# Kernel tuning notes

Hardware: AMD Instinct MI355X
Metric: run time of the kernel (lower is better)

The kernel has to match this reference:

```python
import jax, jax.numpy as jnp
import numpy as np

# Config constants from the W-Net paper (Config() in the original repo)
RADIUS = 5.0
SIGMA_X = 4.0
SIGMA_I = 10.0
PAD = 5  # window offsets dm, dn in [-5, 4] (torch.arange exclusive upper bound)

# Precompute the static list of active window offsets.
# Original: if dist < radius -> w = 0; else w = (dist^2 / -sigma_x) * (||dx|| / -sigma_i)
# (the two negatives cancel, so w = dist^2/sigma_x * ||dx||/sigma_i).
_OFFSETS = []
for dm in range(-5, 5):
    for dn in range(-5, 5):
        d2 = dm * dm + dn * dn
        if np.sqrt(d2) >= RADIUS:  # NOTE: faithful to the (inverted-looking) source condition
            _OFFSETS.append((dm, dn, d2 / SIGMA_X))


def setup_inputs() -> dict:
    key = jax.random.key(0)
    k1, k2 = jax.random.split(key)
    N, K, X, Y, C = 8, 20, 224, 224, 3
    seg = jax.random.uniform(k1, (N, K, X, Y), dtype=jnp.float32)
    x = jax.random.uniform(k2, (N, C, X, Y), dtype=jnp.float32)
    return {"seg": seg, "x": x}


def reference(seg, x):
    N, K, X, Y = seg.shape
    Kconst = jnp.float32(K)
    xi = jnp.transpose(x, (0, 2, 3, 1))  # [N, X, Y, C], matches x[idx].transpose(0,2).transpose(0,1)

    # Zero padding: out-of-window pixels get seg=0, killing their contribution,
    # which exactly reproduces the max(0,.)/min(X,.) loop bounds.
    xp = jnp.pad(xi, ((0, 0), (PAD, PAD), (PAD, PAD), (0, 0)))
    sp = jnp.pad(seg, ((0, 0), (0, 0), (PAD, PAD), (PAD, PAD)))

    # assocA[n,k,i,j] = seg[n,k,i,j] * sum_{dm,dn} w(i,j,i+dm,j+dn) * seg[n,k,i+dm,j+dn]
    accA = jnp.zeros((N, K), dtype=seg.dtype)
    for dm, dn, sw in _OFFSETS:  # static, ~31 offsets
        xs = jax.lax.dynamic_slice(xp, (0, PAD + dm, PAD + dn, 0), (N, X, Y, xi.shape[-1]))
        ss = jax.lax.dynamic_slice(sp, (0, 0, PAD + dm, PAD + dn), (N, K, X, Y))
        diffn = jnp.linalg.norm(xi - xs, axis=-1)  # [N, X, Y], ||xi[i,j]-xi[m,n]||_2
        w = (jnp.float32(sw)) * (diffn / jnp.float32(SIGMA_I))  # [N, X, Y]
        accA = accA + jnp.sum(seg * (w[:, None] * ss), axis=(2, 3))
    assocA_sum = accA  # [N, K]

    # assocV[n,k,i,j] = seg[n,k,i,j] * sum_{m,n'} ||xi[i,j] - xi[m,n']||^2
    # expand: XY*||xi[i,j]||^2 - 2 xi[i,j].S + sum ||xi||^2
    sq = jnp.sum(xi * xi, axis=-1)               # [N, X, Y]
    s2 = jnp.sum(sq, axis=(1, 2))                # [N]
    S = jnp.sum(xi, axis=(1, 2))                 # [N, C]
    npix = jnp.float32(X * Y)
    temp = npix * sq - 2.0 * jnp.einsum('nxyc,nc->nxy', xi, S) + s2[:, None, None]
    assocV_sum = jnp.einsum('nkxy,nxy->nk', seg, temp)  # [N, K]

    Nassoc = assocA_sum / assocV_sum             # [N, K]
    loss = jnp.sum(Kconst - jnp.sum(Nassoc, axis=1))  # sum over batch
    return loss.reshape(1)
```

## Files before the change

kernel.cpp:

```cpp
#include <hip/hip_runtime.h>

#define NB 8
#define KK 20
#define XD 224
#define YD 224
#define NPIX (XD*YD)
#define TILE 16
#define NT 14
#define TW 26
#define NOFF 31
#define NKTOT (NB*KK)
#define NTILES (NT*NT)
#define NPH 2
#define KPH 10
#define SB 32

namespace {
constexpr int DM[NOFF] = {
  -5,-5,-5,-5,-5,-5,-5,-5,-5,-5,
  -4,-4,-4,-4,-4,
  -3,-3,-3,
  -2,-1, 0, 1, 2,
   3, 3, 3,
   4, 4, 4, 4, 4};
constexpr int DN[NOFF] = {
  -5,-4,-3,-2,-1, 0, 1, 2, 3, 4,
  -5,-4,-3, 3, 4,
  -5,-4, 4,
  -5,-5,-5,-5,-5,
  -5,-4, 4,
  -5,-4,-3, 3, 4};

constexpr int ROFXI[NOFF] = {
  (DM[0]+5)*TW+(DN[0]+5),  (DM[1]+5)*TW+(DN[1]+5),  (DM[2]+5)*TW+(DN[2]+5),
  (DM[3]+5)*TW+(DN[3]+5),  (DM[4]+5)*TW+(DN[4]+5),  (DM[5]+5)*TW+(DN[5]+5),
  (DM[6]+5)*TW+(DN[6]+5),  (DM[7]+5)*TW+(DN[7]+5),  (DM[8]+5)*TW+(DN[8]+5),
  (DM[9]+5)*TW+(DN[9]+5),  (DM[10]+5)*TW+(DN[10]+5),(DM[11]+5)*TW+(DN[11]+5),
  (DM[12]+5)*TW+(DN[12]+5),(DM[13]+5)*TW+(DN[13]+5),(DM[14]+5)*TW+(DN[14]+5),
  (DM[15]+5)*TW+(DN[15]+5),(DM[16]+5)*TW+(DN[16]+5),(DM[17]+5)*TW+(DN[17]+5),
  (DM[18]+5)*TW+(DN[18]+5),(DM[19]+5)*TW+(DN[19]+5),(DM[20]+5)*TW+(DN[20]+5),
  (DM[21]+5)*TW+(DN[21]+5),(DM[22]+5)*TW+(DN[22]+5),(DM[23]+5)*TW+(DN[23]+5),
  (DM[24]+5)*TW+(DN[24]+5),(DM[25]+5)*TW+(DN[25]+5),(DM[26]+5)*TW+(DN[26]+5),
  (DM[27]+5)*TW+(DN[27]+5),(DM[28]+5)*TW+(DN[28]+5),(DM[29]+5)*TW+(DN[29]+5),
  (DM[30]+5)*TW+(DN[30]+5)};
constexpr float COSC[NOFF] = {
  (DM[0]*DM[0]+DN[0]*DN[0])/40.0f,   (DM[1]*DM[1]+DN[1]*DN[1])/40.0f,
  (DM[2]*DM[2]+DN[2]*DN[2])/40.0f,   (DM[3]*DM[3]+DN[3]*DN[3])/40.0f,
  (DM[4]*DM[4]+DN[4]*DN[4])/40.0f,   (DM[5]*DM[5]+DN[5]*DN[5])/40.0f,
  (DM[6]*DM[6]+DN[6]*DN[6])/40.0f,   (DM[7]*DM[7]+DN[7]*DN[7])/40.0f,
  (DM[8]*DM[8]+DN[8]*DN[8])/40.0f,   (DM[9]*DM[9]+DN[9]*DN[9])/40.0f,
  (DM[10]*DM[10]+DN[10]*DN[10])/40.0f,(DM[11]*DM[11]+DN[11]*DN[11])/40.0f,
  (DM[12]*DM[12]+DN[12]*DN[12])/40.0f,(DM[13]*DM[13]+DN[13]*DN[13])/40.0f,
  (DM[14]*DM[14]+DN[14]*DN[14])/40.0f,(DM[15]*DM[15]+DN[15]*DN[15])/40.0f,
  (DM[16]*DM[16]+DN[16]*DN[16])/40.0f,(DM[17]*DM[17]+DN[17]*DN[17])/40.0f,
  (DM[18]*DM[18]+DN[18]*DN[18])/40.0f,(DM[19]*DM[19]+DN[19]*DN[19])/40.0f,
  (DM[20]*DM[20]+DN[20]*DN[20])/40.0f,(DM[21]*DM[21]+DN[21]*DN[21])/40.0f,
  (DM[22]*DM[22]+DN[22]*DN[22])/40.0f,(DM[23]*DM[23]+DN[23]*DN[23])/40.0f,
  (DM[24]*DM[24]+DN[24]*DN[24])/40.0f,(DM[25]*DM[25]+DN[25]*DN[25])/40.0f,
  (DM[26]*DM[26]+DN[26]*DN[26])/40.0f,(DM[27]*DM[27]+DN[27]*DN[27])/40.0f,
  (DM[28]*DM[28]+DN[28]*DN[28])/40.0f,(DM[29]*DM[29]+DN[29]*DN[29])/40.0f,
  (DM[30]*DM[30]+DN[30]*DN[30])/40.0f};
}

__global__ void ncuts_stats1(const float* __restrict__ x, float* __restrict__ part) {
  __shared__ float red[4][4];
  const int b = blockIdx.x;
  const int n = b >> 5, s = b & 31;
  const int t = threadIdx.x;
  const int lane = t & 63, wv = t >> 6;
  const float* xb = x + n * 3 * NPIX;
  const int base = s * (NPIX / SB);
  float a0 = 0.f, a1 = 0.f, a2 = 0.f, aq = 0.f;
  for (int i = t; i < NPIX / SB; i += 256) {
    const int p = base + i;
    float v0 = xb[p], v1 = xb[NPIX + p], v2 = xb[2 * NPIX + p];
    a0 += v0; a1 += v1; a2 += v2;
    aq = fmaf(v0, v0, fmaf(v1, v1, fmaf(v2, v2, aq)));
  }
  #pragma unroll
  for (int m = 1; m < 64; m <<= 1) {
    a0 += __shfl_xor(a0, m, 64); a1 += __shfl_xor(a1, m, 64);
    a2 += __shfl_xor(a2, m, 64); aq += __shfl_xor(aq, m, 64);
  }
  if (lane == 0) { red[wv][0] = a0; red[wv][1] = a1; red[wv][2] = a2; red[wv][3] = aq; }
  __syncthreads();
  if (t < 4) part[b * 4 + t] = red[0][t] + red[1][t] + red[2][t] + red[3][t];
}

__global__ void ncuts_stats2(const float* __restrict__ part,
                             float* __restrict__ Sv, float* __restrict__ s2v) {
  const int t = threadIdx.x;
  if (t < NB * 4) {
    const int n = t >> 2, val = t & 3;
    float s = 0.f;
    #pragma unroll 4
    for (int i = 0; i < SB; ++i) s += part[(n * SB + i) * 4 + val];
    if (val < 3) Sv[n * 3 + val] = s; else s2v[n] = s;
  }
}

__global__ __launch_bounds__(256, 4)
void ncuts_main(const float* __restrict__ seg, const float* __restrict__ x,
                const float* __restrict__ Sv, const float* __restrict__ s2v,
                float* __restrict__ pA, float* __restrict__ pV) {
  __shared__ __align__(16) float sSegA[TW*TW*4];
  __shared__ __align__(16) float sSegB[TW*TW*4];
  __shared__ __align__(16) float sSegC[TW*TW*2];
  __shared__ __align__(16) float sXi[TW*TW*4];
  __shared__ float sRed[4][2*KK];

  const int t = threadIdx.x;
  const int lane = t & 63, wv = t >> 6;
  const int tx = t & 15, ty = t >> 4;
  const int tcx = blockIdx.x, tcy = blockIdx.y, n = blockIdx.z;
  const int r0 = tcy * TILE - 5, c0 = tcx * TILE - 5;

  const float* xb = x + n * 3 * NPIX;
  for (int e = t; e < TW * TW; e += 256) {
    const int rr = e / TW, cc = e - rr * TW;
    const int gr = r0 + rr, gc = c0 + cc;
    float v0 = 0.f, v1 = 0.f, v2 = 0.f;
    if ((unsigned)gr < XD && (unsigned)gc < YD) {
      const int g = gr * YD + gc;
      v0 = xb[g]; v1 = xb[NPIX + g]; v2 = xb[2 * NPIX + g];
    }
    *reinterpret_cast<float4*>(&sXi[e * 4]) = make_float4(v0, v1, v2, 0.f);
  }

  const float* sb = seg + n * KK * NPIX;
  const float* psb[3]; bool pok[3];
  #pragma unroll
  for (int s = 0; s < 3; ++s) {
    const int p = t + s * 256;
    const int rr = p / TW, cc = p - rr * TW;
    const int gr = r0 + rr, gc = c0 + cc;
    pok[s] = (p < TW * TW) && ((unsigned)gr < XD) && ((unsigned)gc < YD);
    psb[s] = sb + (gr * YD + gc);
  }

  const int xib = ty * TW + tx;
  const int cen = xib + (5 * TW + 5);

  const float S0 = Sv[n*3+0], S1 = Sv[n*3+1], S2 = Sv[n*3+2], s2n = s2v[n];

  __syncthreads();
  const float4 xc = *reinterpret_cast<const float4*>(&sXi[cen * 4]);
  const float xc0 = xc.x, xc1 = xc.y, xc2 = xc.z;
  const float sqc = xc0*xc0 + xc1*xc1 + xc2*xc2;
  const float temp = 50176.f * sqc - 2.f * (xc0*S0 + xc1*S1 + xc2*S2) + s2n;

  #pragma unroll 1
  for (int p = 0; p < NPH; ++p) {
    const int kbase = p * KPH;

    __syncthreads();

    #pragma unroll
    for (int s = 0; s < 3; ++s) {
      const int pix = t + s * 256;
      if (pix < TW * TW) {
        float v[KPH];
        #pragma unroll
        for (int ks = 0; ks < KPH; ++ks) v[ks] = 0.f;
        if (pok[s]) {
          #pragma unroll
          for (int ks = 0; ks < KPH; ++ks) v[ks] = psb[s][(kbase + ks) * NPIX];
        }
        *reinterpret_cast<float4*>(&sSegA[pix * 4]) = make_float4(v[0], v[1], v[2], v[3]);
        *reinterpret_cast<float4*>(&sSegB[pix * 4]) = make_float4(v[4], v[5], v[6], v[7]);
        *reinterpret_cast<float2*>(&sSegC[pix * 2]) = make_float2(v[8], v[9]);
      }
    }
    __syncthreads();

    float acc[KPH];
    #pragma unroll
    for (int k = 0; k < KPH; ++k) acc[k] = 0.f;

    #pragma unroll 2
    for (int o = 0; o < NOFF; ++o) {
      const int rof = ROFXI[o];
      const float4 xs = *reinterpret_cast<const float4*>(&sXi[(xib + rof) * 4]);
      const float d0 = xc0 - xs.x, d1 = xc1 - xs.y, d2 = xc2 - xs.z;
      const float dd = fmaf(d0, d0, fmaf(d1, d1, d2 * d2));
      const float w = COSC[o] * dd * __frsqrt_rn(fmaxf(dd, 1e-30f));
      const float4 q0 = *reinterpret_cast<const float4*>(&sSegA[(xib + rof) * 4]);
      const float4 q1 = *reinterpret_cast<const float4*>(&sSegB[(xib + rof) * 4]);
      const float2 q2 = *reinterpret_cast<const float2*>(&sSegC[(xib + rof) * 2]);
      acc[0] = fmaf(w, q0.x, acc[0]); acc[1] = fmaf(w, q0.y, acc[1]);
      acc[2] = fmaf(w, q0.z, acc[2]); acc[3] = fmaf(w, q0.w, acc[3]);
      acc[4] = fmaf(w, q1.x, acc[4]); acc[5] = fmaf(w, q1.y, acc[5]);
      acc[6] = fmaf(w, q1.z, acc[6]); acc[7] = fmaf(w, q1.w, acc[7]);
      acc[8] = fmaf(w, q2.x, acc[8]); acc[9] = fmaf(w, q2.y, acc[9]);
    }

    const float4 c0v = *reinterpret_cast<const float4*>(&sSegA[cen * 4]);
    const float4 c1v = *reinterpret_cast<const float4*>(&sSegB[cen * 4]);
    const float2 c2v = *reinterpret_cast<const float2*>(&sSegC[cen * 2]);
    const float segc[KPH] = {c0v.x, c0v.y, c0v.z, c0v.w,
                             c1v.x, c1v.y, c1v.z, c1v.w, c2v.x, c2v.y};

    #pragma unroll
    for (int pp = 0; pp < KPH / 2; ++pp) {
      const int s0i = 2 * pp, s1i = 2 * pp + 1;
      float pa0 = segc[s0i] * acc[s0i], pv0 = segc[s0i] * temp;
      float pa1 = segc[s1i] * acc[s1i], pv1 = segc[s1i] * temp;
      float s0 = (lane & 1) ? pv0 : pa0;
      float g0 = (lane & 1) ? pa0 : pv0;
      s0 += __shfl_xor(g0, 1, 64);
      float s1 = (lane & 1) ? pv1 : pa1;
      float g1 = (lane & 1) ? pa1 : pv1;
      s1 += __shfl_xor(g1, 1, 64);
      float cv = (lane & 2) ? s1 : s0;
      float gv = (lane & 2) ? s0 : s1;
      cv += __shfl_xor(gv, 2, 64);
      cv += __shfl_xor(cv, 4, 64);
      cv += __shfl_xor(cv, 8, 64);
      cv += __shfl_xor(cv, 16, 64);
      cv += __shfl_xor(cv, 32, 64);
      const int k0g = kbase + 2 * pp;
      if (lane < 4) sRed[wv][2 * k0g + lane] = cv;
    }
  }

  __syncthreads();
  if (t < 2 * KK) {
    const float s = sRed[0][t] + sRed[1][t] + sRed[2][t] + sRed[3][t];
    const int tile = tcy * NT + tcx;
    const int k = t >> 1;
    float* dst = (t & 1) ? pV : pA;
    dst[(n * KK + k) * NTILES + tile] = s;
  }
}

__global__ void ncuts_final1(const float* __restrict__ pA, const float* __restrict__ pV,
                             float* __restrict__ rA, float* __restrict__ rV) {
  const int nk = blockIdx.x, t = threadIdx.x;
  float a = 0.f, v = 0.f;
  for (int j = t; j < NTILES; j += 64) {
    a += pA[nk * NTILES + j];
    v += pV[nk * NTILES + j];
  }
  #pragma unroll
  for (int m = 1; m < 64; m <<= 1) {
    a += __shfl_xor(a, m, 64);
    v += __shfl_xor(v, m, 64);
  }
  if (t == 0) { rA[nk] = a; rV[nk] = v; }
}

__global__ void ncuts_final2(const float* __restrict__ rA, const float* __restrict__ rV,
                             float* __restrict__ out) {
  __shared__ float red[256];
  const int t = threadIdx.x;
  float r = 0.f;
  if (t < NKTOT) r = rA[t] / rV[t];
  red[t] = r;
  __syncthreads();
  for (int s = 128; s > 0; s >>= 1) {
    if (t < s) red[t] += red[t + s];
    __syncthreads();
  }
  if (t == 0) out[0] = (float)NKTOT - red[0];
}

extern "C" void kernel_launch(void* const* d_in, const int* in_sizes, int n_in,
                              void* d_out, int out_size, void* d_ws, size_t ws_size,
                              hipStream_t stream) {
  const float* seg = (const float*)d_in[0];
  const float* x   = (const float*)d_in[1];
  float* ws   = (float*)d_ws;
  float* pA   = ws;
  float* pV   = ws + NKTOT * NTILES;
  float* Sv   = ws + 2 * NKTOT * NTILES;
  float* s2v  = Sv + 24;
  float* part = s2v + 8;
  float* rA   = part + 1024;
  float* rV   = rA + NKTOT;

  ncuts_stats1<<<NB * SB, 256, 0, stream>>>(x, part);
  ncuts_stats2<<<1, 64, 0, stream>>>(part, Sv, s2v);
  dim3 grid(NT, NT, NB);
  ncuts_main<<<grid, 256, 0, stream>>>(seg, x, Sv, s2v, pA, pV);
  ncuts_final1<<<NKTOT, 64, 0, stream>>>(pA, pV, rA, rV);
  ncuts_final2<<<1, 256, 0, stream>>>(rA, rV, (float*)d_out);
}
```

Baseline: 131.8 us.

## Defer assocV via per-pixel moment partials, removing stats pre-pass kernels

Expands the assocV term algebraically so the main kernel no longer needs global image sums beforehand. For each k it emits per-tile moments (seg·acc, seg·sq, seg·x_c, seg), along with per-tile image sums. A single final kernel then combines them into the loss. This drops the two stats kernels and one reduction launch, trading them for 3x more shuffle reductions in the main kernel and a serial 196-step loop per thread in the one-block final kernel.

```diff
diff --git a/kernel.cpp b/kernel.cpp
--- a/kernel.cpp
+++ b/kernel.cpp
@@ -13,7 +13,8 @@
 #define NTILES (NT*NT)
 #define NPH 2
 #define KPH 10
-#define SB 32
+#define NCOMP 6
+#define PSTRIDE (NB*KK*NCOMP)
 
 namespace {
 constexpr int DM[NOFF] = {
@@ -62,52 +63,15 @@
   (DM[30]*DM[30]+DN[30]*DN[30])/40.0f};
 }
 
-__global__ void ncuts_stats1(const float* __restrict__ x, float* __restrict__ part) {
-  __shared__ float red[4][4];
-  const int b = blockIdx.x;
-  const int n = b >> 5, s = b & 31;
-  const int t = threadIdx.x;
-  const int lane = t & 63, wv = t >> 6;
-  const float* xb = x + n * 3 * NPIX;
-  const int base = s * (NPIX / SB);
-  float a0 = 0.f, a1 = 0.f, a2 = 0.f, aq = 0.f;
-  for (int i = t; i < NPIX / SB; i += 256) {
-    const int p = base + i;
-    float v0 = xb[p], v1 = xb[NPIX + p], v2 = xb[2 * NPIX + p];
-    a0 += v0; a1 += v1; a2 += v2;
-    aq = fmaf(v0, v0, fmaf(v1, v1, fmaf(v2, v2, aq)));
-  }
-  #pragma unroll
-  for (int m = 1; m < 64; m <<= 1) {
-    a0 += __shfl_xor(a0, m, 64); a1 += __shfl_xor(a1, m, 64);
-    a2 += __shfl_xor(a2, m, 64); aq += __shfl_xor(aq, m, 64);
-  }
-  if (lane == 0) { red[wv][0] = a0; red[wv][1] = a1; red[wv][2] = a2; red[wv][3] = aq; }
-  __syncthreads();
-  if (t < 4) part[b * 4 + t] = red[0][t] + red[1][t] + red[2][t] + red[3][t];
-}
-
-__global__ void ncuts_stats2(const float* __restrict__ part,
-                             float* __restrict__ Sv, float* __restrict__ s2v) {
-  const int t = threadIdx.x;
-  if (t < NB * 4) {
-    const int n = t >> 2, val = t & 3;
-    float s = 0.f;
-    #pragma unroll 4
-    for (int i = 0; i < SB; ++i) s += part[(n * SB + i) * 4 + val];
-    if (val < 3) Sv[n * 3 + val] = s; else s2v[n] = s;
-  }
-}
-
 __global__ __launch_bounds__(256, 4)
 void ncuts_main(const float* __restrict__ seg, const float* __restrict__ x,
-                const float* __restrict__ Sv, const float* __restrict__ s2v,
-                float* __restrict__ pA, float* __restrict__ pV) {
+                float* __restrict__ part6, float* __restrict__ xstat) {
   __shared__ __align__(16) float sSegA[TW*TW*4];
   __shared__ __align__(16) float sSegB[TW*TW*4];
   __shared__ __align__(16) float sSegC[TW*TW*2];
   __shared__ __align__(16) float sXi[TW*TW*4];
-  __shared__ float sRed[4][2*KK];
+  __shared__ float sRed[4][2*KPH*NCOMP];
+  __shared__ float sRedX[4][4];
 
   const int t = threadIdx.x;
   const int lane = t & 63, wv = t >> 6;
@@ -141,13 +105,32 @@
   const int xib = ty * TW + tx;
   const int cen = xib + (5 * TW + 5);
 
-  const float S0 = Sv[n*3+0], S1 = Sv[n*3+1], S2 = Sv[n*3+2], s2n = s2v[n];
+  auto RED4 = [&](float v0, float v1, float v2, float v3) -> float {
+    float s0 = (lane & 1) ? v1 : v0;
+    float g0 = (lane & 1) ? v0 : v1;
+    s0 += __shfl_xor(g0, 1, 64);
+    float s1 = (lane & 1) ? v3 : v2;
+    float g1 = (lane & 1) ? v2 : v3;
+    s1 += __shfl_xor(g1, 1, 64);
+    float cv = (lane & 2) ? s1 : s0;
+    float gv = (lane & 2) ? s0 : s1;
+    cv += __shfl_xor(gv, 2, 64);
+    cv += __shfl_xor(cv, 4, 64);
+    cv += __shfl_xor(cv, 8, 64);
+    cv += __shfl_xor(cv, 16, 64);
+    cv += __shfl_xor(cv, 32, 64);
+    return cv;
+  };
 
   __syncthreads();
   const float4 xc = *reinterpret_cast<const float4*>(&sXi[cen * 4]);
   const float xc0 = xc.x, xc1 = xc.y, xc2 = xc.z;
   const float sqc = xc0*xc0 + xc1*xc1 + xc2*xc2;
-  const float temp = 50176.f * sqc - 2.f * (xc0*S0 + xc1*S1 + xc2*S2) + s2n;
+
+  {
+    const float cvX = RED4(xc0, xc1, xc2, sqc);
+    if (lane < 4) sRedX[wv][lane] = cvX;
+  }
 
   #pragma unroll 1
   for (int p = 0; p < NPH; ++p) {
@@ -200,62 +183,82 @@
     const float segc[KPH] = {c0v.x, c0v.y, c0v.z, c0v.w,
                              c1v.x, c1v.y, c1v.z, c1v.w, c2v.x, c2v.y};
 
-    #pragma unroll
-    for (int pp = 0; pp < KPH / 2; ++pp) {
-      const int s0i = 2 * pp, s1i = 2 * pp + 1;
-      float pa0 = segc[s0i] * acc[s0i], pv0 = segc[s0i] * temp;
-      float pa1 = segc[s1i] * acc[s1i], pv1 = segc[s1i] * temp;
-      float s0 = (lane & 1) ? pv0 : pa0;
-      float g0 = (lane & 1) ? pa0 : pv0;
-      s0 += __shfl_xor(g0, 1, 64);
-      float s1 = (lane & 1) ? pv1 : pa1;
-      float g1 = (lane & 1) ? pa1 : pv1;
-      s1 += __shfl_xor(g1, 1, 64);
-      float cv = (lane & 2) ? s1 : s0;
-      float gv = (lane & 2) ? s0 : s1;
-      cv += __shfl_xor(gv, 2, 64);
-      cv += __shfl_xor(cv, 4, 64);
-      cv += __shfl_xor(cv, 8, 64);
-      cv += __shfl_xor(cv, 16, 64);
-      cv += __shfl_xor(cv, 32, 64);
-      const int k0g = kbase + 2 * pp;
-      if (lane < 4) sRed[wv][2 * k0g + lane] = cv;
-    }
-  }
-
-  __syncthreads();
-  if (t < 2 * KK) {
+    auto VAL = [&](int i) -> float {
+      const int k = i / NCOMP, c = i % NCOMP;
+      const float s = segc[k];
+      return c == 0 ? s * acc[k]
+           : c == 1 ? s * sqc
+           : c == 2 ? s * xc0
+           : c == 3 ? s * xc1
+           : c == 4 ? s * xc2
+           : s;
+    };
+    #pragma unroll
+    for (int jq = 0; jq < (KPH * NCOMP) / 4; ++jq) {
+      const int i0 = 4 * jq;
+      const float cv = RED4(VAL(i0), VAL(i0 + 1), VAL(i0 + 2), VAL(i0 + 3));
+      if (lane < 4) sRed[wv][p * (KPH * NCOMP) + i0 + lane] = cv;
+    }
+  }
+
+  __syncthreads();
+  const int tile = tcy * NT + tcx;
+  if (t < 2 * KPH * NCOMP) {
     const float s = sRed[0][t] + sRed[1][t] + sRed[2][t] + sRed[3][t];
-    const int tile = tcy * NT + tcx;
-    const int k = t >> 1;
-    float* dst = (t & 1) ? pV : pA;
-    dst[(n * KK + k) * NTILES + tile] = s;
-  }
-}
-
-__global__ void ncuts_final1(const float* __restrict__ pA, const float* __restrict__ pV,
-                             float* __restrict__ rA, float* __restrict__ rV) {
-  const int nk = blockIdx.x, t = threadIdx.x;
-  float a = 0.f, v = 0.f;
-  for (int j = t; j < NTILES; j += 64) {
-    a += pA[nk * NTILES + j];
-    v += pV[nk * NTILES + j];
-  }
-  #pragma unroll
-  for (int m = 1; m < 64; m <<= 1) {
-    a += __shfl_xor(a, m, 64);
-    v += __shfl_xor(v, m, 64);
-  }
-  if (t == 0) { rA[nk] = a; rV[nk] = v; }
-}
-
-__global__ void ncuts_final2(const float* __restrict__ rA, const float* __restrict__ rV,
-                             float* __restrict__ out) {
+    part6[tile * PSTRIDE + n * (KK * NCOMP) + t] = s;
+  } else if (t < 2 * KPH * NCOMP + 4) {
+    const int j = t - 2 * KPH * NCOMP;
+    xstat[(n * NTILES + tile) * 4 + j] =
+        sRedX[0][j] + sRedX[1][j] + sRedX[2][j] + sRedX[3][j];
+  }
+}
+
+__global__ void ncuts_final(const float* __restrict__ part6,
+                            const float* __restrict__ xstat,
+                            float* __restrict__ out) {
+  __shared__ float sXr[32][8];
+  __shared__ float sS[NB][4];
+  __shared__ float sP[PSTRIDE];
   __shared__ float red[256];
   const int t = threadIdx.x;
+
+  float s6 = 0.f;
+  if (t < PSTRIDE) {
+    for (int j = 0; j < NTILES; ++j) s6 += part6[j * PSTRIDE + t];
+  }
+  if (t < 256) {
+    const int combo = t >> 3, sub = t & 7;
+    const int n = combo >> 2, j = combo & 3;
+    float s = 0.f;
+    for (int i = sub; i < NTILES; i += 8) s += xstat[(n * NTILES + i) * 4 + j];
+    sXr[combo][sub] = s;
+  }
+  if (t < PSTRIDE) sP[t] = s6;
+  __syncthreads();
+  if (t < 32) {
+    float s = 0.f;
+    #pragma unroll
+    for (int u = 0; u < 8; ++u) s += sXr[t][u];
+    sS[t >> 2][t & 3] = s;
+  }
+  __syncthreads();
+
   float r = 0.f;
-  if (t < NKTOT) r = rA[t] / rV[t];
-  red[t] = r;
+  if (t < NKTOT) {
+    const int n = t / KK;
+    const float pa   = sP[t * 6 + 0];
+    const float psq  = sP[t * 6 + 1];
+    const float px0  = sP[t * 6 + 2];
+    const float px1  = sP[t * 6 + 3];
+    const float px2  = sP[t * 6 + 4];
+    const float pseg = sP[t * 6 + 5];
+    const float S0 = sS[n][0], S1 = sS[n][1], S2 = sS[n][2], s2n = sS[n][3];
+    const float pv = 50176.f * psq
+                   - 2.f * (S0 * px0 + S1 * px1 + S2 * px2)
+                   + s2n * pseg;
+    r = pa / pv;
+  }
+  if (t < 256) red[t] = r;
   __syncthreads();
   for (int s = 128; s > 0; s >>= 1) {
     if (t < s) red[t] += red[t + s];
@@ -269,19 +272,11 @@
                               hipStream_t stream) {
   const float* seg = (const float*)d_in[0];
   const float* x   = (const float*)d_in[1];
-  float* ws   = (float*)d_ws;
-  float* pA   = ws;
-  float* pV   = ws + NKTOT * NTILES;
-  float* Sv   = ws + 2 * NKTOT * NTILES;
-  float* s2v  = Sv + 24;
-  float* part = s2v + 8;
-  float* rA   = part + 1024;
-  float* rV   = rA + NKTOT;
-
-  ncuts_stats1<<<NB * SB, 256, 0, stream>>>(x, part);
-  ncuts_stats2<<<1, 64, 0, stream>>>(part, Sv, s2v);
+  float* ws    = (float*)d_ws;
+  float* part6 = ws;
+  float* xstat = ws + NTILES * PSTRIDE;
+
   dim3 grid(NT, NT, NB);
-  ncuts_main<<<grid, 256, 0, stream>>>(seg, x, Sv, s2v, pA, pV);
-  ncuts_final1<<<NKTOT, 64, 0, stream>>>(pA, pV, rA, rV);
-  ncuts_final2<<<1, 256, 0, stream>>>(rA, rV, (float*)d_out);
-}
+  ncuts_main<<<grid, 256, 0, stream>>>(seg, x, part6, xstat);
+  ncuts_final<<<1, 1024, 0, stream>>>(part6, xstat, (float*)d_out);
+}
```

After: 152.7 us. +15.9%, slower.
